# Optimization experiments

Measured on AMD Instinct MI355X. Metric: run time of the kernel, lower is better.

Reference implementation:

```python
import jax, jax.numpy as jnp
import numpy as np

B, H, V, A, NANN, DEPTH = 32, 256, 512, 3, 8, 7


def preorder_perm(arity, depth):
    # level-order node index -> pre-order position permutation for a full arity-ary tree
    starts = np.cumsum([0] + [arity ** l for l in range(depth + 1)])
    order = []
    def rec(l, p):
        order.append(int(starts[l] + p))
        if l < depth:
            for c in range(arity):
                rec(l + 1, p * arity + c)
    rec(0, 0)
    return np.asarray(order, dtype=np.int32)


def setup_inputs() -> dict:
    key = jax.random.key(0)
    ks = jax.random.split(key, 12)
    s = 0.05
    return {
        "root_hiddens": jax.random.normal(ks[0], (B, H), jnp.float32),
        "ann_table": jax.random.normal(ks[1], (NANN, H), jnp.float32),
        "w1": jax.random.normal(ks[2], (2 * H, H), jnp.float32) * s,
        "b1": jnp.zeros((2 * H,), jnp.float32),
        "w2": jax.random.normal(ks[3], (V, 2 * H), jnp.float32) * s,
        "b2": jnp.zeros((V,), jnp.float32),
        "gru_w_ih": jax.random.normal(ks[4], (A, 3 * H, H), jnp.float32) * s,
        "gru_w_hh": jax.random.normal(ks[5], (A, 3 * H, H), jnp.float32) * s,
        "gru_b_ih": jnp.zeros((A, 3 * H), jnp.float32),
        "gru_b_hh": jnp.zeros((A, 3 * H), jnp.float32),
        "ann_ids": jax.random.randint(ks[6], (B,), 0, NANN, jnp.int32),
        "depth": DEPTH,
    }


def _forward(root_hiddens, ann_table, w1, b1, w2, b2,
             gru_w_ih, gru_w_hh, gru_b_ih, gru_b_hh, ann_ids, depth):
    b, h = root_hiddens.shape
    arity = gru_w_ih.shape[0]
    x = ann_table[ann_ids]                                   # [B,H] annotation embedding (GRU input at every node)
    # input-side gates are constant across the whole tree: precompute once
    gx = jnp.einsum('bh,agh->bag', x, gru_w_ih) + gru_b_ih   # [B,A,3H]
    xr, xz, xn = jnp.split(gx, 3, axis=-1)                   # each [B,A,H]

    hid = root_hiddens[:, None, :]                           # [B,1,H]
    levels = [hid]
    for _ in range(depth):
        gh = jnp.einsum('bnh,agh->bnag', hid, gru_w_hh) + gru_b_hh  # [B,n,A,3H]
        hr, hz, hn = jnp.split(gh, 3, axis=-1)
        r = jax.nn.sigmoid(xr[:, None] + hr)
        z = jax.nn.sigmoid(xz[:, None] + hz)
        n = jnp.tanh(xn[:, None] + r * hn)
        new_h = (1.0 - z) * n + z * hid[:, :, None, :]       # [B,n,A,H]
        hid = new_h.reshape(b, -1, h)                        # child c of node p -> p*A+c
        levels.append(hid)

    all_h = jnp.concatenate(levels, axis=1)                  # [B,N,H] level-order
    mid = jax.nn.sigmoid(jnp.einsum('bnh,oh->bno', all_h, w1) + b1)
    prod = jnp.einsum('bno,vo->bnv', mid, w2) + b2           # [B,N,V]
    perm = jnp.asarray(preorder_perm(arity, depth))
    return jnp.transpose(prod[:, perm, :], (1, 0, 2))        # [N,B,V] (seq-first, like pad_sequence)


def reference(root_hiddens, ann_table, w1, b1, w2, b2,
              gru_w_ih, gru_w_hh, gru_b_ih, gru_b_hh, ann_ids, depth):
    return _forward(root_hiddens, ann_table, w1, b1, w2, b2,
                    gru_w_ih, gru_w_hh, gru_b_ih, gru_b_hh, ann_ids, depth)
```

## Files before the change

### kernel.cpp

```cpp
#include <hip/hip_runtime.h>
#include <hip/hip_bf16.h>
#include <stdint.h>
#include <stddef.h>

#define NB 32
#define NH 256
#define NMID 512
#define NV 512
#define NA 3
#define NDEPTH 7
#define NNODES 3280
#define NG 2304
#define MROWS (NNODES * NB)
#define HM 64

typedef __attribute__((ext_vector_type(8))) short bf16x8;
typedef __attribute__((ext_vector_type(4))) float f32x4;

__device__ __forceinline__ unsigned short f2bf(float x) {
    union { float f; unsigned u; } v; v.f = x;
    unsigned r = v.u + 0x7fffu + ((v.u >> 16) & 1u);
    return (unsigned short)(r >> 16);
}
__device__ __forceinline__ unsigned cvt_pk_bf16(float a, float b) {
    unsigned r;
    asm("v_cvt_pk_bf16_f32 %0, %1, %2" : "=v"(r) : "v"(a), "v"(b));
    return r;
}
__device__ __forceinline__ float bf2f(unsigned short u) {
    union { unsigned u; float f; } v; v.u = ((unsigned)u) << 16;
    return v.f;
}
__device__ __forceinline__ float sigm(float x) { return 1.0f / (1.0f + __expf(-x)); }
__device__ __forceinline__ float tanh_(float x) {
    x = fminf(fmaxf(x, -15.0f), 15.0f);
    float e = __expf(2.0f * x);
    return (e - 1.0f) / (e + 1.0f);
}
__device__ __forceinline__ f32x4 splat4(float s) { f32x4 v = {s, s, s, s}; return v; }

__global__ void cast_weights(const float* __restrict__ whh, const float* __restrict__ w1,
                             const float* __restrict__ w2,
                             unsigned short* __restrict__ whh_b,
                             unsigned short* __restrict__ w1_b,
                             unsigned short* __restrict__ w2_b) {
    const int n_whh = NG * NH;
    const int n_w1  = NMID * NH;
    const int n_w2  = NV * NMID;
    const int total = n_whh + n_w1 + n_w2;
    for (int i = blockIdx.x * blockDim.x + threadIdx.x; i < total;
         i += gridDim.x * blockDim.x) {
        if (i < n_whh) whh_b[i] = f2bf(whh[i]);
        else if (i < n_whh + n_w1) w1_b[i - n_whh] = f2bf(w1[i - n_whh]);
        else w2_b[i - n_whh - n_w1] = f2bf(w2[i - n_whh - n_w1]);
    }
}

__global__ void gx_kernel(const float* __restrict__ ann_table, const int* __restrict__ ann_ids,
                          const float* __restrict__ w_ih, const float* __restrict__ b_ih,
                          float* __restrict__ gx_t) {
    int gw = blockIdx.x * (blockDim.x >> 6) + (threadIdx.x >> 6);
    int lane = threadIdx.x & 63;
    if (gw >= NB * NG) return;
    int b = gw / NG;
    int col = gw - b * NG;
    const float* xr = ann_table + (size_t)ann_ids[b] * NH;
    const float* wr = w_ih + (size_t)col * NH;
    float4 xv = *(const float4*)(xr + lane * 4);
    float4 wv = *(const float4*)(wr + lane * 4);
    float s = xv.x * wv.x + xv.y * wv.y + xv.z * wv.z + xv.w * wv.w;
    #pragma unroll
    for (int off = 32; off; off >>= 1) s += __shfl_down(s, off);
    if (lane == 0) gx_t[(size_t)col * NB + b] = s + b_ih[col];
}

__global__ void init_root(const float* __restrict__ root, unsigned short* __restrict__ hid_b) {
    int i = blockIdx.x * blockDim.x + threadIdx.x;
    if (i < NB * NH) hid_b[i] = f2bf(root[i]);
}

__global__ void posmap_kernel(int* __restrict__ posmap) {
    int n = blockIdx.x * blockDim.x + threadIdx.x;
    if (n >= NNODES) return;
    int start = 0, cnt = 1, l = 0;
    while (n >= start + cnt) { start += cnt; cnt *= 3; l++; }
    int p = n - start;
    int pw = 1;
    for (int j = 0; j < l - 1; j++) pw *= 3;
    int pos = 0;
    for (int k = 1; k <= l; k++) {
        int d = (p / pw) % 3;
        int e = NDEPTH - k + 1;
        int p3 = 1; for (int j = 0; j < e; j++) p3 *= 3;
        pos += 1 + d * ((p3 - 1) / 2);
        pw /= 3;
    }
    posmap[n] = pos;
}

template<int NPB>
__global__ __launch_bounds__(512, 2)
void gru_level(const unsigned short* __restrict__ hid_b_in,
               unsigned short* __restrict__ hid_b_out,
               const unsigned short* __restrict__ whh_b,
               const float* __restrict__ b_hh, const float* __restrict__ gx_t,
               int start, int child_start, int cnt) {
    constexpr int M = 32 * NPB;
    __shared__ char a_s[M * 512];

    int tid = threadIdx.x;
    int lane = tid & 63;
    int wv = tid >> 6;
    int lr = lane & 15;
    int kg = (lane >> 4) * 8;
    int rbase = (lane >> 4) * 4;
    int nrel0 = blockIdx.x * NPB;
    size_t prow0 = (size_t)(start + nrel0) * NB;

    for (int c = tid; c < M * 32; c += 512) {
        int row = c >> 5;
        int coloff = (c & 31) * 8;
        bf16x8 v = *(const bf16x8*)(hid_b_in + (prow0 + row) * NH + coloff);
        *(bf16x8*)(a_s + ((row * 512 + coloff * 2) ^ ((row & 15) << 4))) = v;
    }
    __syncthreads();

    int Gb = (blockIdx.y * 8 + wv) * 16;
    int a = Gb >> 8;
    int colh = (Gb & 255) + lr;
    int gcol = a * 768 + colh;
    const unsigned short* bptr = whh_b + (size_t)(a * 512 + Gb + lr) * NH + kg;

    float bhr = b_hh[gcol], bhz = b_hh[gcol + 256], bhn = b_hh[gcol + 512];

    f32x4 acc[3][2 * NPB];
    #pragma unroll
    for (int g = 0; g < 2; ++g) {
        f32x4 gr = *(const f32x4*)(gx_t + (size_t)gcol * NB + g * 16 + rbase);
        f32x4 gz = *(const f32x4*)(gx_t + (size_t)(gcol + 256) * NB + g * 16 + rbase);
        #pragma unroll
        for (int mi = g; mi < 2 * NPB; mi += 2) {
            acc[0][mi] = gr + splat4(bhr);
            acc[1][mi] = gz + splat4(bhz);
            acc[2][mi] = splat4(bhn);
        }
    }

    bf16x8 bcur[3];
    #pragma unroll
    for (int t = 0; t < 3; ++t) bcur[t] = *(const bf16x8*)(bptr + t * 256 * NH);
    #pragma unroll
    for (int k0 = 0; k0 < NH; k0 += 32) {
        bf16x8 bnxt[3];
        if (k0 + 32 < NH) {
            #pragma unroll
            for (int t = 0; t < 3; ++t) bnxt[t] = *(const bf16x8*)(bptr + t * 256 * NH + k0 + 32);
        }
        bf16x8 af[2 * NPB];
        #pragma unroll
        for (int mi = 0; mi < 2 * NPB; ++mi) {
            int row = mi * 16 + lr;
            af[mi] = *(const bf16x8*)(a_s + ((row * 512 + (k0 + kg) * 2) ^ ((row & 15) << 4)));
        }
        #pragma unroll
        for (int t = 0; t < 3; ++t)
            #pragma unroll
            for (int mi = 0; mi < 2 * NPB; ++mi)
                acc[t][mi] = __builtin_amdgcn_mfma_f32_16x16x32_bf16(af[mi], bcur[t], acc[t][mi], 0, 0, 0);
        if (k0 + 32 < NH) {
            #pragma unroll
            for (int t = 0; t < 3; ++t) bcur[t] = bnxt[t];
        }
    }

    f32x4 gxn[2];
    #pragma unroll
    for (int g = 0; g < 2; ++g)
        gxn[g] = *(const f32x4*)(gx_t + (size_t)(gcol + 512) * NB + g * 16 + rbase);
    #pragma unroll
    for (int mi = 0; mi < 2 * NPB; ++mi) {
        int ns = (mi * 16 + rbase) >> 5;
        if (nrel0 + ns >= cnt) continue;
        size_t crow = ((size_t)(child_start + (nrel0 + ns) * 3 + a)) * NB;
        float hnew[4];
        #pragma unroll
        for (int j = 0; j < 4; ++j) {
            int row = mi * 16 + rbase + j;
            float r = sigm(acc[0][mi][j]);
            float z = sigm(acc[1][mi][j]);
            float nn = tanh_(gxn[mi & 1][j] + r * acc[2][mi][j]);
            unsigned short hpu = *(const unsigned short*)(a_s + ((row * 512 + colh * 2) ^ ((row & 15) << 4)));
            hnew[j] = (1.0f - z) * nn + z * bf2f(hpu);
        }
        unsigned u01 = cvt_pk_bf16(hnew[0], hnew[1]);
        unsigned u23 = cvt_pk_bf16(hnew[2], hnew[3]);
        int b0 = (mi * 16 + rbase) & 31;
        hid_b_out[(crow + b0 + 0) * NH + colh] = (unsigned short)u01;
        hid_b_out[(crow + b0 + 1) * NH + colh] = (unsigned short)(u01 >> 16);
        hid_b_out[(crow + b0 + 2) * NH + colh] = (unsigned short)u23;
        hid_b_out[(crow + b0 + 3) * NH + colh] = (unsigned short)(u23 >> 16);
    }
}

__global__ __launch_bounds__(512, 4)
void head_fused(const unsigned short* __restrict__ hid_b,
                const unsigned short* __restrict__ w1_b, const float* __restrict__ b1,
                const unsigned short* __restrict__ w2_b, const float* __restrict__ b2,
                const int* __restrict__ posmap, float* __restrict__ out) {
    __shared__ char smem[HM * NMID * 2];

    int tid = threadIdx.x;
    int lane = tid & 63;
    int wv = tid >> 6;
    int mbase = blockIdx.x * HM;
    int lr = lane & 15;
    int kg = (lane >> 4) * 8;
    int rbase = (lane >> 4) * 4;
    int n0w = wv * 64;

    for (int c = tid; c < HM * 32; c += 512) {
        int row = c >> 5;
        int coloff = (c & 31) * 8;
        bf16x8 v = *(const bf16x8*)(hid_b + ((size_t)(mbase + row)) * NH + coloff);
        *(bf16x8*)(smem + ((row * 512 + coloff * 2) ^ ((row & 15) << 4))) = v;
    }
    __syncthreads();

    f32x4 acc[4][4];
    #pragma unroll
    for (int mi = 0; mi < 4; ++mi)
        #pragma unroll
        for (int ni = 0; ni < 4; ++ni) acc[mi][ni] = (f32x4){0.f, 0.f, 0.f, 0.f};

    {
        const unsigned short* bbase = w1_b + ((size_t)(n0w + lr)) * NH + kg;
        bf16x8 bcur[4];
        #pragma unroll
        for (int ni = 0; ni < 4; ++ni) bcur[ni] = *(const bf16x8*)(bbase + ni * 16 * NH);
        #pragma unroll
        for (int k0 = 0; k0 < NH; k0 += 32) {
            bf16x8 bnxt[4];
            if (k0 + 32 < NH) {
                #pragma unroll
                for (int ni = 0; ni < 4; ++ni) bnxt[ni] = *(const bf16x8*)(bbase + ni * 16 * NH + k0 + 32);
            }
            bf16x8 af[4];
            #pragma unroll
            for (int mi = 0; mi < 4; ++mi) {
                int row = mi * 16 + lr;
                af[mi] = *(const bf16x8*)(smem + ((row * 512 + (k0 + kg) * 2) ^ ((row & 15) << 4)));
            }
            #pragma unroll
            for (int mi = 0; mi < 4; ++mi)
                #pragma unroll
                for (int ni = 0; ni < 4; ++ni)
                    acc[mi][ni] = __builtin_amdgcn_mfma_f32_16x16x32_bf16(af[mi], bcur[ni], acc[mi][ni], 0, 0, 0);
            if (k0 + 32 < NH) {
                #pragma unroll
                for (int ni = 0; ni < 4; ++ni) bcur[ni] = bnxt[ni];
            }
        }
    }
    __syncthreads();

    #pragma unroll
    for (int mi = 0; mi < 4; ++mi)
        #pragma unroll
        for (int ni = 0; ni < 4; ++ni) {
            int col = n0w + ni * 16 + lr;
            float bv = b1[col];
            float v0 = sigm(acc[mi][ni][0] + bv);
            float v1 = sigm(acc[mi][ni][1] + bv);
            float v2 = sigm(acc[mi][ni][2] + bv);
            float v3 = sigm(acc[mi][ni][3] + bv);
            unsigned u01 = cvt_pk_bf16(v0, v1);
            unsigned u23 = cvt_pk_bf16(v2, v3);
            int r0 = mi * 16 + rbase;
            *(unsigned short*)(smem + (((r0 + 0) * 1024 + col * 2) ^ (((r0 + 0) & 15) << 4))) = (unsigned short)u01;
            *(unsigned short*)(smem + (((r0 + 1) * 1024 + col * 2) ^ (((r0 + 1) & 15) << 4))) = (unsigned short)(u01 >> 16);
            *(unsigned short*)(smem + (((r0 + 2) * 1024 + col * 2) ^ (((r0 + 2) & 15) << 4))) = (unsigned short)u23;
            *(unsigned short*)(smem + (((r0 + 3) * 1024 + col * 2) ^ (((r0 + 3) & 15) << 4))) = (unsigned short)(u23 >> 16);
        }
    __syncthreads();

    #pragma unroll
    for (int mi = 0; mi < 4; ++mi)
        #pragma unroll
        for (int ni = 0; ni < 4; ++ni) acc[mi][ni] = (f32x4){0.f, 0.f, 0.f, 0.f};
    {
        const unsigned short* bbase = w2_b + ((size_t)(n0w + lr)) * NMID + kg;
        bf16x8 bcur[4];
        #pragma unroll
        for (int ni = 0; ni < 4; ++ni) bcur[ni] = *(const bf16x8*)(bbase + ni * 16 * NMID);
        #pragma unroll
        for (int k0 = 0; k0 < NMID; k0 += 32) {
            bf16x8 bnxt[4];
            if (k0 + 32 < NMID) {
                #pragma unroll
                for (int ni = 0; ni < 4; ++ni) bnxt[ni] = *(const bf16x8*)(bbase + ni * 16 * NMID + k0 + 32);
            }
            bf16x8 af[4];
            #pragma unroll
            for (int mi = 0; mi < 4; ++mi) {
                int row = mi * 16 + lr;
                af[mi] = *(const bf16x8*)(smem + ((row * 1024 + (k0 + kg) * 2) ^ ((row & 15) << 4)));
            }
            #pragma unroll
            for (int mi = 0; mi < 4; ++mi)
                #pragma unroll
                for (int ni = 0; ni < 4; ++ni)
                    acc[mi][ni] = __builtin_amdgcn_mfma_f32_16x16x32_bf16(af[mi], bcur[ni], acc[mi][ni], 0, 0, 0);
            if (k0 + 32 < NMID) {
                #pragma unroll
                for (int ni = 0; ni < 4; ++ni) bcur[ni] = bnxt[ni];
            }
        }
    }
    float bv4[4];
    #pragma unroll
    for (int ni = 0; ni < 4; ++ni) bv4[ni] = b2[n0w + ni * 16 + lr];
    #pragma unroll
    for (int mi = 0; mi < 4; ++mi) {
        int row0 = mbase + mi * 16 + rbase;
        #pragma unroll
        for (int j = 0; j < 4; ++j) {
            int row = row0 + j;
            int b = row & 31;
            int node = row >> 5;
            float* orow = out + ((size_t)posmap[node] * NB + b) * NV + n0w + lr;
            #pragma unroll
            for (int ni = 0; ni < 4; ++ni)
                orow[ni * 16] = acc[mi][ni][j] + bv4[ni];
        }
    }
}

extern "C" void kernel_launch(void* const* d_in, const int* in_sizes, int n_in,
                              void* d_out, int out_size, void* d_ws, size_t ws_size,
                              hipStream_t stream) {
    const float* root      = (const float*)d_in[0];
    const float* ann_table = (const float*)d_in[1];
    const float* w1        = (const float*)d_in[2];
    const float* b1        = (const float*)d_in[3];
    const float* w2        = (const float*)d_in[4];
    const float* b2        = (const float*)d_in[5];
    const float* w_ih      = (const float*)d_in[6];
    const float* w_hh      = (const float*)d_in[7];
    const float* b_ih      = (const float*)d_in[8];
    const float* b_hh      = (const float*)d_in[9];
    const int*   ann_ids   = (const int*)d_in[10];

    uint8_t* ws = (uint8_t*)d_ws;
    unsigned short* whh_b = (unsigned short*)ws; ws += (size_t)NG * NH * 2;
    unsigned short* w1_b  = (unsigned short*)ws; ws += (size_t)NMID * NH * 2;
    unsigned short* w2_b  = (unsigned short*)ws; ws += (size_t)NV * NMID * 2;
    float* gx_t           = (float*)ws;          ws += (size_t)NB * NG * 4;
    int* posmap           = (int*)ws;            ws += (size_t)NNODES * 4;
    unsigned short* hid_b = (unsigned short*)ws; ws += (size_t)NNODES * NB * NH * 2;

    cast_weights<<<512, 256, 0, stream>>>(w_hh, w1, w2, whh_b, w1_b, w2_b);
    gx_kernel<<<(NB * NG) / 4, 256, 0, stream>>>(ann_table, ann_ids, w_ih, b_ih, gx_t);
    init_root<<<(NB * NH + 255) / 256, 256, 0, stream>>>(root, hid_b);
    posmap_kernel<<<(NNODES + 255) / 256, 256, 0, stream>>>(posmap);

    int start = 0, cnt = 1;
    for (int l = 0; l < NDEPTH; ++l) {
        int child_start = start + cnt;
        if (cnt >= 243) {
            gru_level<4><<<dim3((cnt + 3) / 4, 6), 512, 0, stream>>>(
                hid_b, hid_b, whh_b, b_hh, gx_t, start, child_start, cnt);
        } else {
            gru_level<1><<<dim3(cnt, 6), 512, 0, stream>>>(
                hid_b, hid_b, whh_b, b_hh, gx_t, start, child_start, cnt);
        }
        start = child_start; cnt *= 3;
    }
    head_fused<<<MROWS / HM, 512, 0, stream>>>(hid_b, w1_b, b1, w2_b, b2, posmap, (float*)d_out);
}
```

Measured before the change: 380.9 us.

## Fuse prep kernels into one launch and stage head output through LDS

The four small setup kernels (weight casting, input-gate precompute, root init, pre-order map) are merged into one grid-stride kernel to cut launch overhead. The head epilogue now writes accumulators into swizzled shared memory, one node (32 rows) at a time. It then emits full contiguous 2 KB rows per node with 16-byte vector stores, replacing scattered 4-byte stores. This targets the cost of writing the large output, at the price of extra barriers and LDS traffic in the epilogue.

```diff
diff --git a/kernel.cpp b/kernel.cpp
--- a/kernel.cpp
+++ b/kernel.cpp
@@ -39,49 +39,7 @@
 }
 __device__ __forceinline__ f32x4 splat4(float s) { f32x4 v = {s, s, s, s}; return v; }
 
-__global__ void cast_weights(const float* __restrict__ whh, const float* __restrict__ w1,
-                             const float* __restrict__ w2,
-                             unsigned short* __restrict__ whh_b,
-                             unsigned short* __restrict__ w1_b,
-                             unsigned short* __restrict__ w2_b) {
-    const int n_whh = NG * NH;
-    const int n_w1  = NMID * NH;
-    const int n_w2  = NV * NMID;
-    const int total = n_whh + n_w1 + n_w2;
-    for (int i = blockIdx.x * blockDim.x + threadIdx.x; i < total;
-         i += gridDim.x * blockDim.x) {
-        if (i < n_whh) whh_b[i] = f2bf(whh[i]);
-        else if (i < n_whh + n_w1) w1_b[i - n_whh] = f2bf(w1[i - n_whh]);
-        else w2_b[i - n_whh - n_w1] = f2bf(w2[i - n_whh - n_w1]);
-    }
-}
-
-__global__ void gx_kernel(const float* __restrict__ ann_table, const int* __restrict__ ann_ids,
-                          const float* __restrict__ w_ih, const float* __restrict__ b_ih,
-                          float* __restrict__ gx_t) {
-    int gw = blockIdx.x * (blockDim.x >> 6) + (threadIdx.x >> 6);
-    int lane = threadIdx.x & 63;
-    if (gw >= NB * NG) return;
-    int b = gw / NG;
-    int col = gw - b * NG;
-    const float* xr = ann_table + (size_t)ann_ids[b] * NH;
-    const float* wr = w_ih + (size_t)col * NH;
-    float4 xv = *(const float4*)(xr + lane * 4);
-    float4 wv = *(const float4*)(wr + lane * 4);
-    float s = xv.x * wv.x + xv.y * wv.y + xv.z * wv.z + xv.w * wv.w;
-    #pragma unroll
-    for (int off = 32; off; off >>= 1) s += __shfl_down(s, off);
-    if (lane == 0) gx_t[(size_t)col * NB + b] = s + b_ih[col];
-}
-
-__global__ void init_root(const float* __restrict__ root, unsigned short* __restrict__ hid_b) {
-    int i = blockIdx.x * blockDim.x + threadIdx.x;
-    if (i < NB * NH) hid_b[i] = f2bf(root[i]);
-}
-
-__global__ void posmap_kernel(int* __restrict__ posmap) {
-    int n = blockIdx.x * blockDim.x + threadIdx.x;
-    if (n >= NNODES) return;
+__device__ __forceinline__ int preorder_pos(int n) {
     int start = 0, cnt = 1, l = 0;
     while (n >= start + cnt) { start += cnt; cnt *= 3; l++; }
     int p = n - start;
@@ -95,7 +53,44 @@
         pos += 1 + d * ((p3 - 1) / 2);
         pw /= 3;
     }
-    posmap[n] = pos;
+    return pos;
+}
+
+__global__ void prep_all(const float* __restrict__ root, const float* __restrict__ ann_table,
+                         const int* __restrict__ ann_ids,
+                         const float* __restrict__ w_ih, const float* __restrict__ b_ih,
+                         const float* __restrict__ whh_f, const float* __restrict__ w1_f,
+                         const float* __restrict__ w2_f,
+                         unsigned short* __restrict__ whh_b, unsigned short* __restrict__ w1_b,
+                         unsigned short* __restrict__ w2_b,
+                         float* __restrict__ gx_t, int* __restrict__ posmap,
+                         unsigned short* __restrict__ hid_b) {
+    int gtid = blockIdx.x * blockDim.x + threadIdx.x;
+    int nth = gridDim.x * blockDim.x;
+    const int n_whh = NG * NH, n_w1 = NMID * NH, n_w2 = NV * NMID;
+    const int total = n_whh + n_w1 + n_w2;
+    for (int i = gtid; i < total; i += nth) {
+        if (i < n_whh) whh_b[i] = f2bf(whh_f[i]);
+        else if (i < n_whh + n_w1) w1_b[i - n_whh] = f2bf(w1_f[i - n_whh]);
+        else w2_b[i - n_whh - n_w1] = f2bf(w2_f[i - n_whh - n_w1]);
+    }
+    if (gtid < NB * NH) hid_b[gtid] = f2bf(root[gtid]);
+    if (gtid < NNODES) posmap[gtid] = preorder_pos(gtid);
+    int lane = threadIdx.x & 63;
+    int gw = gtid >> 6;
+    int nw = nth >> 6;
+    for (int e = gw; e < NB * NG; e += nw) {
+        int b = e / NG;
+        int col = e - b * NG;
+        const float* xr = ann_table + (size_t)ann_ids[b] * NH;
+        const float* wr = w_ih + (size_t)col * NH;
+        float4 xv = *(const float4*)(xr + lane * 4);
+        float4 wv = *(const float4*)(wr + lane * 4);
+        float s = xv.x * wv.x + xv.y * wv.y + xv.z * wv.z + xv.w * wv.w;
+        #pragma unroll
+        for (int off = 32; off; off >>= 1) s += __shfl_down(s, off);
+        if (lane == 0) gx_t[(size_t)col * NB + b] = s + b_ih[col];
+    }
 }
 
 template<int NPB>
@@ -316,22 +311,40 @@
             }
         }
     }
+    __syncthreads();
+
     float bv4[4];
     #pragma unroll
     for (int ni = 0; ni < 4; ++ni) bv4[ni] = b2[n0w + ni * 16 + lr];
     #pragma unroll
-    for (int mi = 0; mi < 4; ++mi) {
-        int row0 = mbase + mi * 16 + rbase;
-        #pragma unroll
-        for (int j = 0; j < 4; ++j) {
-            int row = row0 + j;
-            int b = row & 31;
-            int node = row >> 5;
-            float* orow = out + ((size_t)posmap[node] * NB + b) * NV + n0w + lr;
-            #pragma unroll
-            for (int ni = 0; ni < 4; ++ni)
-                orow[ni * 16] = acc[mi][ni][j] + bv4[ni];
-        }
+    for (int h = 0; h < 2; ++h) {
+        #pragma unroll
+        for (int mm = 0; mm < 2; ++mm) {
+            int mi = h * 2 + mm;
+            #pragma unroll
+            for (int ni = 0; ni < 4; ++ni) {
+                int col = n0w + ni * 16 + lr;
+                #pragma unroll
+                for (int j = 0; j < 4; ++j) {
+                    int rl = mm * 16 + rbase + j;
+                    int byteoff = (rl * 2048 + col * 4) ^ ((rl & 7) << 4);
+                    *(float*)(smem + byteoff) = acc[mi][ni][j] + bv4[ni];
+                }
+            }
+        }
+        __syncthreads();
+        int pos = posmap[blockIdx.x * 2 + h];
+        float* obase = out + (size_t)pos * NB * NV;
+        #pragma unroll
+        for (int i = 0; i < 8; ++i) {
+            int f = tid + i * 512;
+            int rl = f >> 7;
+            int cq = f & 127;
+            int byteoff = (rl * 2048 + cq * 16) ^ ((rl & 7) << 4);
+            f32x4 v = *(const f32x4*)(smem + byteoff);
+            *(f32x4*)(obase + (size_t)rl * NV + cq * 4) = v;
+        }
+        if (h == 0) __syncthreads();
     }
 }
 
@@ -358,10 +371,9 @@
     int* posmap           = (int*)ws;            ws += (size_t)NNODES * 4;
     unsigned short* hid_b = (unsigned short*)ws; ws += (size_t)NNODES * NB * NH * 2;
 
-    cast_weights<<<512, 256, 0, stream>>>(w_hh, w1, w2, whh_b, w1_b, w2_b);
-    gx_kernel<<<(NB * NG) / 4, 256, 0, stream>>>(ann_table, ann_ids, w_ih, b_ih, gx_t);
-    init_root<<<(NB * NH + 255) / 256, 256, 0, stream>>>(root, hid_b);
-    posmap_kernel<<<(NNODES + 255) / 256, 256, 0, stream>>>(posmap);
+    prep_all<<<1024, 256, 0, stream>>>(root, ann_table, ann_ids, w_ih, b_ih,
+                                       w_hh, w1, w2, whh_b, w1_b, w2_b,
+                                       gx_t, posmap, hid_b);
 
     int start = 0, cnt = 1;
     for (int l = 0; l < NDEPTH; ++l) {
```

Result: no change. 377.6 us (-0.9%).
